# Kernel optimization log

Measured on AMD Instinct MI355X. Metric: run time of the kernel, lower is better.

The kernel has to match this reference:

```python
import jax, jax.numpy as jnp
import numpy as np

D_MODEL = 768
D_INNER = 1536      # d_model * expand
D_STATE = 128
D_CONV = 4
HEADDIM = 64
NHEADS = 24         # d_inner / headdim
CONV_DIM = D_INNER + 2 * D_STATE          # 1792
D_IN_PROJ = 2 * D_INNER + 2 * D_STATE + NHEADS  # 3352
EPS = 1e-5
BATCH, SEQLEN = 4, 2048


def setup_inputs() -> dict:
    key = jax.random.key(0)
    ks = jax.random.split(key, 8)
    u = jax.random.normal(ks[0], (BATCH, SEQLEN, D_MODEL), dtype=jnp.float32)
    W_in = jax.random.normal(ks[1], (D_IN_PROJ, D_MODEL), dtype=jnp.float32) * 0.02
    conv_w = jax.random.normal(ks[2], (CONV_DIM, D_CONV), dtype=jnp.float32) * 0.2
    conv_b = jnp.zeros((CONV_DIM,), dtype=jnp.float32)
    # dt_bias = inverse-softplus of dt sampled log-uniformly in [dt_min, dt_max]
    dt = jnp.exp(jax.random.uniform(ks[3], (NHEADS,)) * (np.log(0.1) - np.log(0.001)) + np.log(0.001))
    dt = jnp.clip(dt, 1e-4, None)
    dt_bias = dt + jnp.log(-jnp.expm1(-dt))
    A_log = jnp.log(jax.random.uniform(ks[4], (NHEADS,), minval=1.0, maxval=16.0))
    D = jnp.ones((NHEADS,), dtype=jnp.float32)
    norm_w = jnp.ones((D_INNER,), dtype=jnp.float32)
    W_out = jax.random.normal(ks[5], (D_MODEL, D_INNER), dtype=jnp.float32) * 0.02
    return {"u": u, "W_in": W_in, "conv_w": conv_w, "conv_b": conv_b,
            "dt_bias": dt_bias, "A_log": A_log, "D": D, "norm_w": norm_w, "W_out": W_out}


def reference(u, W_in, conv_w, conv_b, dt_bias, A_log, D, norm_w, W_out):
    b, L, _ = u.shape
    zxbcdt = jnp.einsum('bld,ed->ble', u, W_in)  # (b, L, 3352)
    z = zxbcdt[..., :D_INNER]
    xBC = zxbcdt[..., D_INNER:D_INNER + CONV_DIM]
    dt = zxbcdt[..., D_INNER + CONV_DIM:]        # (b, L, nheads)

    # causal depthwise conv1d (kernel width 4), then SiLU
    xp = jnp.pad(xBC, ((0, 0), (D_CONV - 1, 0), (0, 0)))
    xBC = sum(xp[:, k:k + L, :] * conv_w[:, k] for k in range(D_CONV)) + conv_b
    xBC = jax.nn.silu(xBC)

    x = xBC[..., :D_INNER].reshape(b, L, NHEADS, HEADDIM)
    B = xBC[..., D_INNER:D_INNER + D_STATE]      # (b, L, n)  (ngroups=1)
    C = xBC[..., D_INNER + D_STATE:]             # (b, L, n)

    dt = jax.nn.softplus(dt + dt_bias)           # (b, L, h)
    A = -jnp.exp(A_log)                          # (h,)
    dA = jnp.exp(dt * A)                         # (b, L, h)

    def step(h, inp):
        dA_t, dt_t, x_t, B_t, C_t = inp
        # h: (b, h, p, n)
        h = h * dA_t[:, :, None, None] + jnp.einsum('bhp,bh,bn->bhpn', x_t, dt_t, B_t)
        y = jnp.einsum('bhpn,bn->bhp', h, C_t)
        return h, y

    xs = (jnp.swapaxes(dA, 0, 1), jnp.swapaxes(dt, 0, 1), jnp.swapaxes(x, 0, 1),
          jnp.swapaxes(B, 0, 1), jnp.swapaxes(C, 0, 1))
    h0 = jnp.zeros((b, NHEADS, HEADDIM, D_STATE), dtype=u.dtype)
    _, ys = jax.lax.scan(step, h0, xs)           # ys: (L, b, h, p)
    y = jnp.swapaxes(ys, 0, 1)                   # (b, L, h, p)

    y = y + D[None, None, :, None] * x           # skip connection
    y = y.reshape(b, L, D_INNER)

    # RMSNorm then gate with silu(z)
    y = norm_w * y * jax.lax.rsqrt(jnp.mean(y * y, axis=-1, keepdims=True) + EPS)
    y = y * jax.nn.silu(z)
    return jnp.einsum('bld,ed->ble', y, W_out)
```

## Files before the change

kernel.cpp:

```cpp
#include <hip/hip_runtime.h>
#include <hip/hip_bf16.h>

typedef __bf16 bf16x8 __attribute__((ext_vector_type(8)));
typedef float f32x4 __attribute__((ext_vector_type(4)));
typedef unsigned int u32x4 __attribute__((ext_vector_type(4)));

#define MTOT    8192
#define DMODEL  768
#define DINNER  1536
#define DSTATE  128
#define NHEADS  24
#define CONVDIM 1792
#define LDZ     3328
#define SEQ     2048
#define CHUNK   128
#define NCHUNK  16
#define NBH     96

#define NU   (MTOT*DMODEL)
#define NWI  (LDZ*DMODEL)
#define NWO  (DMODEL*DINNER)
#define NWD  (32*DMODEL)

__device__ __forceinline__ void gl2lds16(const __hip_bfloat16* g, __hip_bfloat16* l) {
  __builtin_amdgcn_global_load_lds((const __attribute__((address_space(1))) void*)g,
                                   (__attribute__((address_space(3))) void*)l, 16, 0, 0);
}

__global__ __launch_bounds__(256) void cvt_bf16(const float* __restrict__ u, const float* __restrict__ Wi,
                                                const float* __restrict__ Wo,
                                                __hip_bfloat16* __restrict__ ub, __hip_bfloat16* __restrict__ wib,
                                                __hip_bfloat16* __restrict__ wob,
                                                __hip_bfloat16* __restrict__ wdh, __hip_bfloat16* __restrict__ wdl) {
  int i = blockIdx.x * 256 + threadIdx.x;
  if (i < NU) ub[i] = __float2bfloat16(u[i]);
  else if (i < NU + NWI) { int k = i - NU; wib[k] = __float2bfloat16(Wi[k]); }
  else if (i < NU + NWI + NWO) { int k = i - NU - NWI; wob[k] = __float2bfloat16(Wo[k]); }
  else if (i < NU + NWI + NWO + 2 * NWD) {
    int k = i - NU - NWI - NWO;
    int lo = (k >= NWD);
    if (lo) k -= NWD;
    int row = k / DMODEL, col = k - row * DMODEL;
    float w = (row < NHEADS) ? Wi[(size_t)(LDZ + row) * DMODEL + col] : 0.f;
    __hip_bfloat16 h = __float2bfloat16(w);
    if (!lo) wdh[k] = h;
    else wdl[k] = __float2bfloat16(w - __bfloat162float(h));
  }
}

__global__ __launch_bounds__(256, 2) void gemm_bt(const __hip_bfloat16* __restrict__ A,
                                                  const __hip_bfloat16* __restrict__ B,
                                                  float* __restrict__ C, int lda, int ldb, int ldc, int nk) {
  __shared__ __align__(16) __hip_bfloat16 As[128 * 32];
  __shared__ __align__(16) __hip_bfloat16 Bs[128 * 32];
  const int tid = threadIdx.x;
  const int lane = tid & 63, wid = tid >> 6;
  const int wm = wid >> 1, wn = wid & 1;
  const int bm = blockIdx.y, bn = blockIdx.x;
  const int sr = (lane >> 2), sc = (lane & 3) * 8;
  const __hip_bfloat16* Ag0 = A + (size_t)(bm * 128 + wid * 32 + sr) * lda + sc;
  const __hip_bfloat16* Ag1 = Ag0 + (size_t)16 * lda;
  const __hip_bfloat16* Bg0 = B + (size_t)(bn * 128 + wid * 32 + sr) * ldb + sc;
  const __hip_bfloat16* Bg1 = Bg0 + (size_t)16 * ldb;
  __hip_bfloat16* Al0 = &As[(wid * 32) * 32];
  __hip_bfloat16* Al1 = &As[(wid * 32 + 16) * 32];
  __hip_bfloat16* Bl0 = &Bs[(wid * 32) * 32];
  __hip_bfloat16* Bl1 = &Bs[(wid * 32 + 16) * 32];
  f32x4 acc[4][4] = {};
  const int lr = lane & 15, lk = lane >> 4;
  const int arow = wm * 64 + lr, brow = wn * 64 + lr;
  for (int ks = 0; ks < nk; ++ks) {
    gl2lds16(Ag0 + ks * 32, Al0);
    gl2lds16(Ag1 + ks * 32, Al1);
    gl2lds16(Bg0 + ks * 32, Bl0);
    gl2lds16(Bg1 + ks * 32, Bl1);
    __syncthreads();
    bf16x8 af[4], bfr[4];
#pragma unroll
    for (int i = 0; i < 4; ++i) {
      af[i] = *(const bf16x8*)&As[(arow + i * 16) * 32 + lk * 8];
      bfr[i] = *(const bf16x8*)&Bs[(brow + i * 16) * 32 + lk * 8];
    }
#pragma unroll
    for (int i = 0; i < 4; ++i)
#pragma unroll
      for (int j = 0; j < 4; ++j)
        acc[i][j] = __builtin_amdgcn_mfma_f32_16x16x32_bf16(af[i], bfr[j], acc[i][j], 0, 0, 0);
    __syncthreads();
  }
  const int crow0 = bm * 128 + wm * 64 + lk * 4;
  const int ccol0 = bn * 128 + wn * 64 + lr;
#pragma unroll
  for (int i = 0; i < 4; ++i)
#pragma unroll
    for (int j = 0; j < 4; ++j)
#pragma unroll
      for (int r = 0; r < 4; ++r)
        C[(size_t)(crow0 + i * 16 + r) * ldc + ccol0 + j * 16] = acc[i][j][r];
}

__global__ __launch_bounds__(256) void dt_mfma(const float* __restrict__ u,
                                               const __hip_bfloat16* __restrict__ wdh,
                                               const __hip_bfloat16* __restrict__ wdl,
                                               const float* __restrict__ dtb, const float* __restrict__ alog,
                                               float* __restrict__ dtS, float* __restrict__ dtA) {
  __shared__ __align__(16) __hip_bfloat16 Uh[64 * 32];
  __shared__ __align__(16) __hip_bfloat16 Ul[64 * 32];
  const int tid = threadIdx.x;
  const int lane = tid & 63, wid = tid >> 6;
  const int lr = lane & 15, lk = lane >> 4;
  const int bm = blockIdx.x;
  const int r = tid >> 2, c0 = (tid & 3) * 8;
  const float* usrc = u + (size_t)(bm * 64 + r) * DMODEL + c0;
  f32x4 acc[2] = {};
  for (int ks = 0; ks < DMODEL / 32; ++ks) {
    float4 v0 = *(const float4*)(usrc + ks * 32);
    float4 v1 = *(const float4*)(usrc + ks * 32 + 4);
    bf16x8 hi, lo;
    const float* vf = (const float*)&v0;
#pragma unroll
    for (int e = 0; e < 4; ++e) {
      __hip_bfloat16 h = __float2bfloat16(vf[e]);
      hi[e] = *(__bf16*)&h;
      __hip_bfloat16 l2 = __float2bfloat16(vf[e] - __bfloat162float(h));
      lo[e] = *(__bf16*)&l2;
    }
    vf = (const float*)&v1;
#pragma unroll
    for (int e = 0; e < 4; ++e) {
      __hip_bfloat16 h = __float2bfloat16(vf[e]);
      hi[4 + e] = *(__bf16*)&h;
      __hip_bfloat16 l2 = __float2bfloat16(vf[e] - __bfloat162float(h));
      lo[4 + e] = *(__bf16*)&l2;
    }
    *(bf16x8*)&Uh[r * 32 + c0] = hi;
    *(bf16x8*)&Ul[r * 32 + c0] = lo;
    __syncthreads();
    bf16x8 ah = *(const bf16x8*)&Uh[(wid * 16 + lr) * 32 + lk * 8];
    bf16x8 al = *(const bf16x8*)&Ul[(wid * 16 + lr) * 32 + lk * 8];
#pragma unroll
    for (int j = 0; j < 2; ++j) {
      bf16x8 bh = *(const bf16x8*)(wdh + (size_t)(j * 16 + lr) * DMODEL + ks * 32 + lk * 8);
      bf16x8 bl = *(const bf16x8*)(wdl + (size_t)(j * 16 + lr) * DMODEL + ks * 32 + lk * 8);
      acc[j] = __builtin_amdgcn_mfma_f32_16x16x32_bf16(ah, bh, acc[j], 0, 0, 0);
      acc[j] = __builtin_amdgcn_mfma_f32_16x16x32_bf16(ah, bl, acc[j], 0, 0, 0);
      acc[j] = __builtin_amdgcn_mfma_f32_16x16x32_bf16(al, bh, acc[j], 0, 0, 0);
    }
    __syncthreads();
  }
#pragma unroll
  for (int j = 0; j < 2; ++j) {
    int col = j * 16 + lr;
    if (col < NHEADS) {
      float nA = -expf(alog[col]);
      float bia = dtb[col];
#pragma unroll
      for (int rr = 0; rr < 4; ++rr) {
        int row = bm * 64 + wid * 16 + lk * 4 + rr;
        float x = acc[j][rr] + bia;
        float dt = (x > 20.f) ? x : log1pf(expf(x));
        dtS[(size_t)row * NHEADS + col] = dt;
        dtA[(size_t)row * NHEADS + col] = nA * dt;
      }
    }
  }
}

__global__ __launch_bounds__(256) void cumsum_kernel(const float* __restrict__ dtA, float* __restrict__ scum,
                                                     float* __restrict__ cdec) {
  int bc = blockIdx.x;
  int b = bc >> 4, c = bc & 15;
  __shared__ float buf[CHUNK * NHEADS];
  int m0 = b * SEQ + c * CHUNK;
  for (int t = threadIdx.x; t < CHUNK * NHEADS; t += 256)
    buf[t] = dtA[(size_t)m0 * NHEADS + t];
  __syncthreads();
  if (threadIdx.x < NHEADS) {
    int h = threadIdx.x;
    float run = 0.f;
    float* dst = scum + ((size_t)bc * NHEADS + h) * CHUNK;
    for (int j = 0; j < CHUNK; ++j) { run += buf[j * NHEADS + h]; dst[j] = run; }
    cdec[(b * NHEADS + h) * NCHUNK + c] = __expf(run);
  }
}

__global__ __launch_bounds__(256) void conv_prep(const float* __restrict__ zxb, const float* __restrict__ cw,
                                                 const float* __restrict__ cb, const float* __restrict__ dtS,
                                                 __hip_bfloat16* __restrict__ Xd, __hip_bfloat16* __restrict__ Bb,
                                                 __hip_bfloat16* __restrict__ Cb) {
  int c = blockIdx.x * 256 + threadIdx.x;
  int m = blockIdx.y;
  int l = m & (SEQ - 1);
  const float* src = zxb + (size_t)m * LDZ + DINNER + c;
  float4 w = *(const float4*)(cw + (size_t)c * 4);
  float acc = cb[c];
#pragma unroll
  for (int k = 0; k < 4; ++k) {
    int ll = l + k - 3;
    if (ll >= 0) acc = fmaf(src[(ptrdiff_t)(k - 3) * LDZ], ((const float*)&w)[k], acc);
  }
  float v = acc / (1.f + __expf(-acc));
  if (c < DINNER) Xd[(size_t)m * DINNER + c] = __float2bfloat16(dtS[m * NHEADS + (c >> 6)] * v);
  else if (c < DINNER + DSTATE) Bb[(size_t)m * DSTATE + (c - DINNER)] = __float2bfloat16(v);
  else Cb[(size_t)m * DSTATE + (c - DINNER - DSTATE)] = __float2bfloat16(v);
}

__global__ __launch_bounds__(256) void transp(const __hip_bfloat16* __restrict__ Xd,
                                              const __hip_bfloat16* __restrict__ Bb,
                                              __hip_bfloat16* __restrict__ XdT, __hip_bfloat16* __restrict__ Bt) {
  __shared__ __hip_bfloat16 t[64][72];
  int bid = blockIdx.x;
  const __hip_bfloat16* src;
  __hip_bfloat16* dst;
  int srcld;
  if (bid < 3072) {
    int tm = bid & 127, tc = bid >> 7;
    int m0 = tm * 64, c0 = tc * 64, b = m0 >> 11;
    src = Xd + (size_t)m0 * DINNER + c0; srcld = DINNER;
    dst = XdT + ((size_t)(b * DINNER + c0)) * SEQ + (m0 - b * SEQ);
  } else {
    int k = bid - 3072;
    int tm = k & 127, tn = k >> 7;
    int m0 = tm * 64, n0 = tn * 64, b = m0 >> 11;
    src = Bb + (size_t)m0 * DSTATE + n0; srcld = DSTATE;
    dst = Bt + ((size_t)(b * DSTATE + n0)) * SEQ + (m0 - b * SEQ);
  }
  int r = threadIdx.x >> 2, cc = (threadIdx.x & 3) * 16;
  *(u32x4*)&t[r][cc] = *(const u32x4*)(src + (size_t)r * srcld + cc);
  *(u32x4*)&t[r][cc + 8] = *(const u32x4*)(src + (size_t)r * srcld + cc + 8);
  __syncthreads();
  __hip_bfloat16 tmp[16] __attribute__((aligned(16)));
#pragma unroll
  for (int k2 = 0; k2 < 16; ++k2) tmp[k2] = t[cc + k2][r];
  *(u32x4*)(dst + (size_t)r * SEQ + cc) = *(u32x4*)&tmp[0];
  *(u32x4*)(dst + (size_t)r * SEQ + cc + 8) = *(u32x4*)&tmp[8];
}

__global__ __launch_bounds__(256, 2) void state_gemm(const __hip_bfloat16* __restrict__ XdT,
                                                     const __hip_bfloat16* __restrict__ Bt,
                                                     const float* __restrict__ scum, float* __restrict__ cstat) {
  __shared__ __align__(16) __hip_bfloat16 Xw[64 * 136];
  __shared__ __align__(16) __hip_bfloat16 Bts[128 * 136];
  __shared__ float rS[CHUNK];
  int bid = blockIdx.x;
  int c = bid & 15, bh = bid >> 4;
  int b = bh / NHEADS, h = bh % NHEADS;
  const float* sp = scum + ((size_t)(b * NCHUNK + c) * NHEADS + h) * CHUNK;
  int tid = threadIdx.x;
  if (tid < CHUNK) rS[tid] = __expf(sp[CHUNK - 1] - sp[tid]);
  {
    int n = tid >> 1, jc = (tid & 1) * 64;
    const __hip_bfloat16* g = Bt + ((size_t)(b * DSTATE + n)) * SEQ + c * CHUNK + jc;
#pragma unroll
    for (int q = 0; q < 8; ++q) *(u32x4*)&Bts[n * 136 + jc + q * 8] = *(const u32x4*)(g + q * 8);
  }
  __syncthreads();
  {
    int p = tid >> 2, jc = (tid & 3) * 32;
    const __hip_bfloat16* g = XdT + ((size_t)((b * NHEADS + h) * 64 + p)) * SEQ + c * CHUNK + jc;
#pragma unroll
    for (int q = 0; q < 4; ++q) {
      bf16x8 vv = *(const bf16x8*)(g + q * 8);
      bf16x8 ov;
#pragma unroll
      for (int e = 0; e < 8; ++e) ov[e] = (__bf16)((float)vv[e] * rS[jc + q * 8 + e]);
      *(bf16x8*)&Xw[p * 136 + jc + q * 8] = ov;
    }
  }
  __syncthreads();
  const int lane = tid & 63, wid = tid >> 6;
  const int wm = wid >> 1, wn = wid & 1;
  const int lr = lane & 15, lk = lane >> 4;
  f32x4 acc[2][4] = {};
#pragma unroll
  for (int ks = 0; ks < 4; ++ks) {
    bf16x8 af[2], bq[4];
#pragma unroll
    for (int i = 0; i < 2; ++i) af[i] = *(const bf16x8*)&Xw[(wm * 32 + i * 16 + lr) * 136 + ks * 32 + lk * 8];
#pragma unroll
    for (int j = 0; j < 4; ++j) bq[j] = *(const bf16x8*)&Bts[(wn * 64 + j * 16 + lr) * 136 + ks * 32 + lk * 8];
#pragma unroll
    for (int i = 0; i < 2; ++i)
#pragma unroll
      for (int j = 0; j < 4; ++j)
        acc[i][j] = __builtin_amdgcn_mfma_f32_16x16x32_bf16(af[i], bq[j], acc[i][j], 0, 0, 0);
  }
  float* dst = cstat + (size_t)bid * 8192;
#pragma unroll
  for (int i = 0; i < 2; ++i)
#pragma unroll
    for (int j = 0; j < 4; ++j)
#pragma unroll
      for (int r = 0; r < 4; ++r)
        dst[(wm * 32 + i * 16 + lk * 4 + r) * 128 + wn * 64 + j * 16 + lr] = acc[i][j][r];
}

__global__ __launch_bounds__(256) void scanB(float* __restrict__ cstat, const float* __restrict__ cdec) {
  const int bh = blockIdx.x >> 3, sl = blockIdx.x & 7;
  const int base = sl * 1024 + threadIdx.x * 4;
  float hreg[4];
#pragma unroll
  for (int j = 0; j < 4; ++j) hreg[j] = 0.f;
  for (int c = 0; c < NCHUNK; ++c) {
    float* p = cstat + (size_t)(bh * NCHUNK + c) * 8192 + base;
    const float P = cdec[bh * NCHUNK + c];
    f32x4 tmp = *(const f32x4*)p;
    f32x4 hs = {hreg[0], hreg[1], hreg[2], hreg[3]};
    *(f32x4*)p = hs;
#pragma unroll
    for (int j = 0; j < 4; ++j) hreg[j] = fmaf(hreg[j], P, tmp[j]);
  }
}

template <int JE>
__global__ __launch_bounds__(256, 2) void ssd_y(const __hip_bfloat16* __restrict__ Cb,
                                                const __hip_bfloat16* __restrict__ Bb,
                                                const __hip_bfloat16* __restrict__ XdT,
                                                const __hip_bfloat16* __restrict__ Xd,
                                                const float* __restrict__ cstat, const float* __restrict__ scum,
                                                const float* __restrict__ dtS, const float* __restrict__ Dvec,
                                                float* __restrict__ zxb) {
  constexpr int HI = JE - 64;
  constexpr int JW = JE / 2;
  constexpr int FJ = JW / 16;
  constexpr int KJ = JE / 32;
  __shared__ __align__(16) __hip_bfloat16 Cs[64 * 136];
  __shared__ __align__(16) __hip_bfloat16 Bs[JE * 136];
  __shared__ __align__(16) __hip_bfloat16 R3[64 * 136];
  __shared__ float sS[CHUNK];
  int bid = blockIdx.x;
  int c = bid & 15, bh = bid >> 4;
  int b = bh / NHEADS, h = bh % NHEADS;
  int m0 = b * SEQ + c * CHUNK;
  int tid = threadIdx.x;
  const float* sp = scum + ((size_t)(b * NCHUNK + c) * NHEADS + h) * CHUNK;
  if (tid < CHUNK) sS[tid] = sp[tid];
  {
    int r = tid >> 2, nc = (tid & 3) * 32;
    const __hip_bfloat16* g = Cb + (size_t)(m0 + HI + r) * DSTATE + nc;
#pragma unroll
    for (int q = 0; q < 4; ++q) *(u32x4*)&Cs[r * 136 + nc + q * 8] = *(const u32x4*)(g + q * 8);
  }
  if (JE == 64) {
    int r = tid >> 2, nc = (tid & 3) * 32;
    const __hip_bfloat16* g = Bb + (size_t)(m0 + r) * DSTATE + nc;
#pragma unroll
    for (int q = 0; q < 4; ++q) *(u32x4*)&Bs[r * 136 + nc + q * 8] = *(const u32x4*)(g + q * 8);
  } else {
    int r = tid >> 1, nc = (tid & 1) * 64;
    const __hip_bfloat16* g = Bb + (size_t)(m0 + r) * DSTATE + nc;
#pragma unroll
    for (int q = 0; q < 8; ++q) *(u32x4*)&Bs[r * 136 + nc + q * 8] = *(const u32x4*)(g + q * 8);
  }
  {
    int p = tid >> 2, nc = (tid & 3) * 32;
    const float* g = cstat + (size_t)bid * 8192 + p * 128 + nc;
#pragma unroll
    for (int q = 0; q < 4; ++q) {
      f32x4 v0 = *(const f32x4*)(g + q * 8);
      f32x4 v1 = *(const f32x4*)(g + q * 8 + 4);
      bf16x8 ov;
      ov[0] = (__bf16)v0[0]; ov[1] = (__bf16)v0[1]; ov[2] = (__bf16)v0[2]; ov[3] = (__bf16)v0[3];
      ov[4] = (__bf16)v1[0]; ov[5] = (__bf16)v1[1]; ov[6] = (__bf16)v1[2]; ov[7] = (__bf16)v1[3];
      *(bf16x8*)&R3[p * 136 + nc + q * 8] = ov;
    }
  }
  __syncthreads();
  const int lane = tid & 63, wid = tid >> 6;
  const int wm = wid >> 1, wn = wid & 1;
  const int lr = lane & 15, lk = lane >> 4;
  f32x4 Gacc[2][FJ] = {};
  f32x4 Uacc[2][2] = {};
#pragma unroll
  for (int ks = 0; ks < 4; ++ks) {
    bf16x8 af[2], bq[2];
#pragma unroll
    for (int i = 0; i < 2; ++i) af[i] = *(const bf16x8*)&Cs[(wm * 32 + i * 16 + lr) * 136 + ks * 32 + lk * 8];
#pragma unroll
    for (int j = 0; j < 2; ++j) bq[j] = *(const bf16x8*)&R3[(wn * 32 + j * 16 + lr) * 136 + ks * 32 + lk * 8];
#pragma unroll
    for (int i = 0; i < 2; ++i)
#pragma unroll
      for (int j = 0; j < 2; ++j)
        Uacc[i][j] = __builtin_amdgcn_mfma_f32_16x16x32_bf16(af[i], bq[j], Uacc[i][j], 0, 0, 0);
  }
#pragma unroll
  for (int ks = 0; ks < 4; ++ks) {
    bf16x8 af[2], bq[FJ];
#pragma unroll
    for (int i = 0; i < 2; ++i) af[i] = *(const bf16x8*)&Cs[(wm * 32 + i * 16 + lr) * 136 + ks * 32 + lk * 8];
#pragma unroll
    for (int j = 0; j < FJ; ++j) bq[j] = *(const bf16x8*)&Bs[(wn * JW + j * 16 + lr) * 136 + ks * 32 + lk * 8];
#pragma unroll
    for (int i = 0; i < 2; ++i)
#pragma unroll
      for (int j = 0; j < FJ; ++j)
        Gacc[i][j] = __builtin_amdgcn_mfma_f32_16x16x32_bf16(af[i], bq[j], Gacc[i][j], 0, 0, 0);
  }
  __syncthreads();
  {
    float siv[2][4];
#pragma unroll
    for (int i = 0; i < 2; ++i)
#pragma unroll
      for (int r = 0; r < 4; ++r) siv[i][r] = sS[HI + wm * 32 + i * 16 + lk * 4 + r];
#pragma unroll
    for (int i = 0; i < 2; ++i)
#pragma unroll
      for (int j = 0; j < FJ; ++j) {
        int gj = wn * JW + j * 16 + lr;
        float sj = sS[gj];
#pragma unroll
        for (int r = 0; r < 4; ++r) {
          int il = wm * 32 + i * 16 + lk * 4 + r;
          int gi = HI + il;
          float mv = (gj <= gi) ? Gacc[i][j][r] * __expf(siv[i][r] - sj) : 0.f;
          Cs[il * 136 + gj] = __float2bfloat16(mv);
        }
      }
  }
  {
    int p = tid >> 2, jc = (tid & 3) * (JE / 4);
    const __hip_bfloat16* g = XdT + ((size_t)((b * NHEADS + h) * 64 + p)) * SEQ + c * CHUNK + jc;
#pragma unroll
    for (int q = 0; q < JE / 32; ++q) *(u32x4*)&R3[p * 136 + jc + q * 8] = *(const u32x4*)(g + q * 8);
  }
  __syncthreads();
  f32x4 Yacc[2][2] = {};
#pragma unroll
  for (int ks = 0; ks < KJ; ++ks) {
    bf16x8 af[2], bq[2];
#pragma unroll
    for (int i = 0; i < 2; ++i) af[i] = *(const bf16x8*)&Cs[(wm * 32 + i * 16 + lr) * 136 + ks * 32 + lk * 8];
#pragma unroll
    for (int j = 0; j < 2; ++j) bq[j] = *(const bf16x8*)&R3[(wn * 32 + j * 16 + lr) * 136 + ks * 32 + lk * 8];
#pragma unroll
    for (int i = 0; i < 2; ++i)
#pragma unroll
      for (int j = 0; j < 2; ++j)
        Yacc[i][j] = __builtin_amdgcn_mfma_f32_16x16x32_bf16(af[i], bq[j], Yacc[i][j], 0, 0, 0);
  }
  const float Dh = Dvec[h];
#pragma unroll
  for (int i = 0; i < 2; ++i)
#pragma unroll
    for (int r = 0; r < 4; ++r) {
      int il = wm * 32 + i * 16 + lk * 4 + r;
      int gi = HI + il;
      int m = m0 + gi;
      float ei = __expf(sS[gi]);
      float dt = dtS[(size_t)m * NHEADS + h];
#pragma unroll
      for (int j = 0; j < 2; ++j) {
        int p = wn * 32 + j * 16 + lr;
        float xv = (float)Xd[(size_t)m * DINNER + h * 64 + p] / dt;
        zxb[(size_t)m * LDZ + DINNER + h * 64 + p] = Yacc[i][j][r] + ei * Uacc[i][j][r] + Dh * xv;
      }
    }
}

__global__ __launch_bounds__(256) void norm_gate(const float* __restrict__ zxb, const float* __restrict__ nw,
                                                 __hip_bfloat16* __restrict__ yg) {
  const int m = blockIdx.x, tid = threadIdx.x;
  const float* zr = zxb + (size_t)m * LDZ;
  const float* yr = zr + DINNER;
  float yv[6], zv[6];
  float ss = 0.f;
#pragma unroll
  for (int jj = 0; jj < 6; ++jj) {
    int i = tid + jj * 256;
    yv[jj] = yr[i];
    zv[jj] = zr[i];
    ss = fmaf(yv[jj], yv[jj], ss);
  }
#pragma unroll
  for (int o = 32; o > 0; o >>= 1) ss += __shfl_down(ss, o);
  __shared__ float red[4];
  if ((tid & 63) == 0) red[tid >> 6] = ss;
  __syncthreads();
  float tot = red[0] + red[1] + red[2] + red[3];
  float r = rsqrtf(tot * (1.f / 1536.f) + 1e-5f);
#pragma unroll
  for (int jj = 0; jj < 6; ++jj) {
    int i = tid + jj * 256;
    float z = zv[jj];
    float g = z / (1.f + __expf(-z));
    yg[(size_t)m * DINNER + i] = __float2bfloat16(nw[i] * yv[jj] * r * g);
  }
}

extern "C" void kernel_launch(void* const* d_in, const int* in_sizes, int n_in,
                              void* d_out, int out_size, void* d_ws, size_t ws_size,
                              hipStream_t stream) {
  (void)in_sizes; (void)n_in; (void)out_size; (void)ws_size;
  const float* u       = (const float*)d_in[0];
  const float* W_in    = (const float*)d_in[1];
  const float* conv_w  = (const float*)d_in[2];
  const float* conv_b  = (const float*)d_in[3];
  const float* dt_bias = (const float*)d_in[4];
  const float* A_log   = (const float*)d_in[5];
  const float* Dvec    = (const float*)d_in[6];
  const float* norm_w  = (const float*)d_in[7];
  const float* W_out   = (const float*)d_in[8];
  float* out = (float*)d_out;

  float* zxb   = (float*)d_ws;
  float* cstat = zxb + (size_t)MTOT * LDZ;
  float* dtS   = cstat + (size_t)NBH * NCHUNK * 8192;
  float* dtA   = dtS + (size_t)MTOT * NHEADS;
  float* scum  = dtA + (size_t)MTOT * NHEADS;
  float* cdec  = scum + (size_t)MTOT * NHEADS;
  __hip_bfloat16* ub  = (__hip_bfloat16*)(cdec + NBH * NCHUNK);
  __hip_bfloat16* wib = ub + (size_t)NU;
  __hip_bfloat16* wob = wib + (size_t)NWI;
  __hip_bfloat16* wdh = wob + (size_t)NWO;
  __hip_bfloat16* wdl = wdh + (size_t)NWD;
  __hip_bfloat16* Xd  = wdl + (size_t)NWD;
  __hip_bfloat16* Bb  = Xd + (size_t)MTOT * DINNER;
  __hip_bfloat16* Cb  = Bb + (size_t)MTOT * DSTATE;
  __hip_bfloat16* XdT = Cb + (size_t)MTOT * DSTATE;
  __hip_bfloat16* Bt  = XdT + (size_t)MTOT * DINNER;
  __hip_bfloat16* yg  = Xd;

  cvt_bf16<<<(NU + NWI + NWO + 2 * NWD + 255) / 256, 256, 0, stream>>>(u, W_in, W_out, ub, wib, wob, wdh, wdl);
  gemm_bt<<<dim3(LDZ / 128, MTOT / 128), 256, 0, stream>>>(ub, wib, zxb, DMODEL, DMODEL, LDZ, DMODEL / 32);
  dt_mfma<<<MTOT / 64, 256, 0, stream>>>(u, wdh, wdl, dt_bias, A_log, dtS, dtA);
  cumsum_kernel<<<64, 256, 0, stream>>>(dtA, scum, cdec);
  conv_prep<<<dim3(CONVDIM / 256, MTOT), 256, 0, stream>>>(zxb, conv_w, conv_b, dtS, Xd, Bb, Cb);
  transp<<<3072 + 256, 256, 0, stream>>>(Xd, Bb, XdT, Bt);
  state_gemm<<<NBH * NCHUNK, 256, 0, stream>>>(XdT, Bt, scum, cstat);
  scanB<<<NBH * 8, 256, 0, stream>>>(cstat, cdec);
  ssd_y<64><<<NBH * NCHUNK, 256, 0, stream>>>(Cb, Bb, XdT, Xd, cstat, scum, dtS, Dvec, zxb);
  ssd_y<128><<<NBH * NCHUNK, 256, 0, stream>>>(Cb, Bb, XdT, Xd, cstat, scum, dtS, Dvec, zxb);
  norm_gate<<<MTOT, 256, 0, stream>>>(zxb, norm_w, yg);
  gemm_bt<<<dim3(DMODEL / 128, MTOT / 128), 256, 0, stream>>>(yg, wob, out, DINNER, DINNER, DMODEL, DINNER / 32);
}
```

Before: 416.7 us.

## Double-buffer GEMM LDS with swizzle, fuse conv with transpose, store chunk states in bf16

The bf16 GEMM now double-buffers its LDS tiles, issuing the next k-step's global-to-LDS loads before the current MFMAs, and XOR-swizzles the tile layout to reduce bank conflicts. The conv/SiLU kernel is merged with the transpose kernel, so each 64x64 tile is computed once, written row-major and transposed from LDS, which removes a launch and a re-read of Xd/Bb. Per-chunk states are stored in bf16 instead of fp32, halving traffic through state_gemm, scanB and ssd_y. The trade-off is extra rounding in the inter-chunk state recurrence, and twice the GEMM LDS footprint, which may limit occupancy.

```diff
diff --git a/kernel.cpp b/kernel.cpp
--- a/kernel.cpp
+++ b/kernel.cpp
@@ -51,35 +51,40 @@
 __global__ __launch_bounds__(256, 2) void gemm_bt(const __hip_bfloat16* __restrict__ A,
                                                   const __hip_bfloat16* __restrict__ B,
                                                   float* __restrict__ C, int lda, int ldb, int ldc, int nk) {
-  __shared__ __align__(16) __hip_bfloat16 As[128 * 32];
-  __shared__ __align__(16) __hip_bfloat16 Bs[128 * 32];
+  __shared__ __align__(16) __hip_bfloat16 As[2][128 * 32];
+  __shared__ __align__(16) __hip_bfloat16 Bs[2][128 * 32];
   const int tid = threadIdx.x;
   const int lane = tid & 63, wid = tid >> 6;
   const int wm = wid >> 1, wn = wid & 1;
   const int bm = blockIdx.y, bn = blockIdx.x;
-  const int sr = (lane >> 2), sc = (lane & 3) * 8;
-  const __hip_bfloat16* Ag0 = A + (size_t)(bm * 128 + wid * 32 + sr) * lda + sc;
+  const int sr = lane >> 2;
+  const int sc = (((lane & 3) ^ ((sr >> 1) & 3))) * 8;
+  const int row0 = wid * 32 + sr;
+  const __hip_bfloat16* Ag0 = A + (size_t)(bm * 128 + row0) * lda + sc;
   const __hip_bfloat16* Ag1 = Ag0 + (size_t)16 * lda;
-  const __hip_bfloat16* Bg0 = B + (size_t)(bn * 128 + wid * 32 + sr) * ldb + sc;
+  const __hip_bfloat16* Bg0 = B + (size_t)(bn * 128 + row0) * ldb + sc;
   const __hip_bfloat16* Bg1 = Bg0 + (size_t)16 * ldb;
-  __hip_bfloat16* Al0 = &As[(wid * 32) * 32];
-  __hip_bfloat16* Al1 = &As[(wid * 32 + 16) * 32];
-  __hip_bfloat16* Bl0 = &Bs[(wid * 32) * 32];
-  __hip_bfloat16* Bl1 = &Bs[(wid * 32 + 16) * 32];
   f32x4 acc[4][4] = {};
   const int lr = lane & 15, lk = lane >> 4;
   const int arow = wm * 64 + lr, brow = wn * 64 + lr;
+  const int ach = (lk ^ ((lr >> 1) & 3)) * 8;
+#define STAGE(buf, ks)                                   \
+  do {                                                   \
+    gl2lds16(Ag0 + (ks) * 32, &As[buf][(wid * 32) * 32]);      \
+    gl2lds16(Ag1 + (ks) * 32, &As[buf][(wid * 32 + 16) * 32]); \
+    gl2lds16(Bg0 + (ks) * 32, &Bs[buf][(wid * 32) * 32]);      \
+    gl2lds16(Bg1 + (ks) * 32, &Bs[buf][(wid * 32 + 16) * 32]); \
+  } while (0)
+  STAGE(0, 0);
+  __syncthreads();
   for (int ks = 0; ks < nk; ++ks) {
-    gl2lds16(Ag0 + ks * 32, Al0);
-    gl2lds16(Ag1 + ks * 32, Al1);
-    gl2lds16(Bg0 + ks * 32, Bl0);
-    gl2lds16(Bg1 + ks * 32, Bl1);
-    __syncthreads();
+    const int cur = ks & 1;
+    if (ks + 1 < nk) STAGE(cur ^ 1, ks + 1);
     bf16x8 af[4], bfr[4];
 #pragma unroll
     for (int i = 0; i < 4; ++i) {
-      af[i] = *(const bf16x8*)&As[(arow + i * 16) * 32 + lk * 8];
-      bfr[i] = *(const bf16x8*)&Bs[(brow + i * 16) * 32 + lk * 8];
+      af[i] = *(const bf16x8*)&As[cur][(arow + i * 16) * 32 + ach];
+      bfr[i] = *(const bf16x8*)&Bs[cur][(brow + i * 16) * 32 + ach];
     }
 #pragma unroll
     for (int i = 0; i < 4; ++i)
@@ -88,6 +93,7 @@
         acc[i][j] = __builtin_amdgcn_mfma_f32_16x16x32_bf16(af[i], bfr[j], acc[i][j], 0, 0, 0);
     __syncthreads();
   }
+#undef STAGE
   const int crow0 = bm * 128 + wm * 64 + lk * 4;
   const int ccol0 = bn * 128 + wn * 64 + lr;
 #pragma unroll
@@ -184,61 +190,59 @@
   }
 }
 
-__global__ __launch_bounds__(256) void conv_prep(const float* __restrict__ zxb, const float* __restrict__ cw,
-                                                 const float* __restrict__ cb, const float* __restrict__ dtS,
-                                                 __hip_bfloat16* __restrict__ Xd, __hip_bfloat16* __restrict__ Bb,
-                                                 __hip_bfloat16* __restrict__ Cb) {
-  int c = blockIdx.x * 256 + threadIdx.x;
-  int m = blockIdx.y;
-  int l = m & (SEQ - 1);
-  const float* src = zxb + (size_t)m * LDZ + DINNER + c;
-  float4 w = *(const float4*)(cw + (size_t)c * 4);
-  float acc = cb[c];
-#pragma unroll
-  for (int k = 0; k < 4; ++k) {
-    int ll = l + k - 3;
-    if (ll >= 0) acc = fmaf(src[(ptrdiff_t)(k - 3) * LDZ], ((const float*)&w)[k], acc);
-  }
-  float v = acc / (1.f + __expf(-acc));
-  if (c < DINNER) Xd[(size_t)m * DINNER + c] = __float2bfloat16(dtS[m * NHEADS + (c >> 6)] * v);
-  else if (c < DINNER + DSTATE) Bb[(size_t)m * DSTATE + (c - DINNER)] = __float2bfloat16(v);
-  else Cb[(size_t)m * DSTATE + (c - DINNER - DSTATE)] = __float2bfloat16(v);
-}
-
-__global__ __launch_bounds__(256) void transp(const __hip_bfloat16* __restrict__ Xd,
-                                              const __hip_bfloat16* __restrict__ Bb,
-                                              __hip_bfloat16* __restrict__ XdT, __hip_bfloat16* __restrict__ Bt) {
+__global__ __launch_bounds__(256) void conv_fused(const float* __restrict__ zxb, const float* __restrict__ cw,
+                                                  const float* __restrict__ cb, const float* __restrict__ dtS,
+                                                  __hip_bfloat16* __restrict__ Xd, __hip_bfloat16* __restrict__ Bb,
+                                                  __hip_bfloat16* __restrict__ Cb, __hip_bfloat16* __restrict__ XdT,
+                                                  __hip_bfloat16* __restrict__ Bt) {
   __shared__ __hip_bfloat16 t[64][72];
-  int bid = blockIdx.x;
-  const __hip_bfloat16* src;
-  __hip_bfloat16* dst;
-  int srcld;
-  if (bid < 3072) {
-    int tm = bid & 127, tc = bid >> 7;
-    int m0 = tm * 64, c0 = tc * 64, b = m0 >> 11;
-    src = Xd + (size_t)m0 * DINNER + c0; srcld = DINNER;
-    dst = XdT + ((size_t)(b * DINNER + c0)) * SEQ + (m0 - b * SEQ);
-  } else {
-    int k = bid - 3072;
-    int tm = k & 127, tn = k >> 7;
-    int m0 = tm * 64, n0 = tn * 64, b = m0 >> 11;
-    src = Bb + (size_t)m0 * DSTATE + n0; srcld = DSTATE;
-    dst = Bt + ((size_t)(b * DSTATE + n0)) * SEQ + (m0 - b * SEQ);
-  }
-  int r = threadIdx.x >> 2, cc = (threadIdx.x & 3) * 16;
-  *(u32x4*)&t[r][cc] = *(const u32x4*)(src + (size_t)r * srcld + cc);
-  *(u32x4*)&t[r][cc + 8] = *(const u32x4*)(src + (size_t)r * srcld + cc + 8);
-  __syncthreads();
-  __hip_bfloat16 tmp[16] __attribute__((aligned(16)));
-#pragma unroll
-  for (int k2 = 0; k2 < 16; ++k2) tmp[k2] = t[cc + k2][r];
-  *(u32x4*)(dst + (size_t)r * SEQ + cc) = *(u32x4*)&tmp[0];
-  *(u32x4*)(dst + (size_t)r * SEQ + cc + 8) = *(u32x4*)&tmp[8];
+  __shared__ float dts_sh[64];
+  const int c0 = blockIdx.x * 64, m0 = blockIdx.y * 64;
+  const int b = m0 >> 11, l0 = m0 & (SEQ - 1);
+  const int tid = threadIdx.x;
+  const int c = tid & 63, rg = tid >> 6;
+  const int gc = c0 + c;
+  const bool isX = (c0 < DINNER);
+  if (isX && tid < 64) dts_sh[tid] = dtS[(size_t)(m0 + tid) * NHEADS + (c0 >> 6)];
+  const float4 w = *(const float4*)(cw + (size_t)gc * 4);
+  const float bias = cb[gc];
+  const float* src = zxb + (size_t)(m0 + rg * 16) * LDZ + DINNER + gc;
+  const int lbase = l0 + rg * 16;
+  float v0 = (lbase >= 3) ? src[-3 * (ptrdiff_t)LDZ] : 0.f;
+  float v1 = (lbase >= 2) ? src[-2 * (ptrdiff_t)LDZ] : 0.f;
+  float v2 = (lbase >= 1) ? src[-1 * (ptrdiff_t)LDZ] : 0.f;
+  __syncthreads();
+#pragma unroll
+  for (int r = 0; r < 16; ++r) {
+    float v3 = src[(ptrdiff_t)r * LDZ];
+    float a = bias + v0 * w.x + v1 * w.y + v2 * w.z + v3 * w.w;
+    float sv = a / (1.f + __expf(-a));
+    int lm = rg * 16 + r;
+    __hip_bfloat16 val = __float2bfloat16(isX ? dts_sh[lm] * sv : sv);
+    t[lm][c] = val;
+    int m = m0 + lm;
+    if (isX) Xd[(size_t)m * DINNER + gc] = val;
+    else if (gc < DINNER + DSTATE) Bb[(size_t)m * DSTATE + gc - DINNER] = val;
+    else Cb[(size_t)m * DSTATE + gc - DINNER - DSTATE] = val;
+    v0 = v1; v1 = v2; v2 = v3;
+  }
+  __syncthreads();
+  if (c0 < DINNER + DSTATE) {
+    int r2 = tid >> 2, cc = (tid & 3) * 16;
+    __hip_bfloat16 tmp[16] __attribute__((aligned(16)));
+#pragma unroll
+    for (int k = 0; k < 16; ++k) tmp[k] = t[cc + k][r2];
+    __hip_bfloat16* dst = isX ? XdT + ((size_t)(b * DINNER + c0 + r2)) * SEQ + l0 + cc
+                              : Bt + ((size_t)(b * DSTATE + (c0 - DINNER) + r2)) * SEQ + l0 + cc;
+    *(u32x4*)dst = *(u32x4*)&tmp[0];
+    *(u32x4*)(dst + 8) = *(u32x4*)&tmp[8];
+  }
 }
 
 __global__ __launch_bounds__(256, 2) void state_gemm(const __hip_bfloat16* __restrict__ XdT,
                                                      const __hip_bfloat16* __restrict__ Bt,
-                                                     const float* __restrict__ scum, float* __restrict__ cstat) {
+                                                     const float* __restrict__ scum,
+                                                     __hip_bfloat16* __restrict__ cstat) {
   __shared__ __align__(16) __hip_bfloat16 Xw[64 * 136];
   __shared__ __align__(16) __hip_bfloat16 Bts[128 * 136];
   __shared__ float rS[CHUNK];
@@ -285,30 +289,30 @@
       for (int j = 0; j < 4; ++j)
         acc[i][j] = __builtin_amdgcn_mfma_f32_16x16x32_bf16(af[i], bq[j], acc[i][j], 0, 0, 0);
   }
-  float* dst = cstat + (size_t)bid * 8192;
+  __hip_bfloat16* dst = cstat + (size_t)bid * 8192;
 #pragma unroll
   for (int i = 0; i < 2; ++i)
 #pragma unroll
     for (int j = 0; j < 4; ++j)
 #pragma unroll
       for (int r = 0; r < 4; ++r)
-        dst[(wm * 32 + i * 16 + lk * 4 + r) * 128 + wn * 64 + j * 16 + lr] = acc[i][j][r];
-}
-
-__global__ __launch_bounds__(256) void scanB(float* __restrict__ cstat, const float* __restrict__ cdec) {
+        dst[(wm * 32 + i * 16 + lk * 4 + r) * 128 + wn * 64 + j * 16 + lr] = __float2bfloat16(acc[i][j][r]);
+}
+
+__global__ __launch_bounds__(256) void scanB(__hip_bfloat16* __restrict__ cstat, const float* __restrict__ cdec) {
   const int bh = blockIdx.x >> 3, sl = blockIdx.x & 7;
   const int base = sl * 1024 + threadIdx.x * 4;
-  float hreg[4];
-#pragma unroll
-  for (int j = 0; j < 4; ++j) hreg[j] = 0.f;
+  float hreg[4] = {0.f, 0.f, 0.f, 0.f};
   for (int c = 0; c < NCHUNK; ++c) {
-    float* p = cstat + (size_t)(bh * NCHUNK + c) * 8192 + base;
+    __hip_bfloat16* p = cstat + (size_t)(bh * NCHUNK + c) * 8192 + base;
     const float P = cdec[bh * NCHUNK + c];
-    f32x4 tmp = *(const f32x4*)p;
-    f32x4 hs = {hreg[0], hreg[1], hreg[2], hreg[3]};
-    *(f32x4*)p = hs;
-#pragma unroll
-    for (int j = 0; j < 4; ++j) hreg[j] = fmaf(hreg[j], P, tmp[j]);
+    __hip_bfloat16 tmp[4], hs[4];
+    *(uint2*)tmp = *(const uint2*)p;
+#pragma unroll
+    for (int j = 0; j < 4; ++j) hs[j] = __float2bfloat16(hreg[j]);
+    *(uint2*)p = *(uint2*)hs;
+#pragma unroll
+    for (int j = 0; j < 4; ++j) hreg[j] = fmaf(hreg[j], P, __bfloat162float(tmp[j]));
   }
 }
 
@@ -317,7 +321,8 @@
                                                 const __hip_bfloat16* __restrict__ Bb,
                                                 const __hip_bfloat16* __restrict__ XdT,
                                                 const __hip_bfloat16* __restrict__ Xd,
-                                                const float* __restrict__ cstat, const float* __restrict__ scum,
+                                                const __hip_bfloat16* __restrict__ cstat,
+                                                const float* __restrict__ scum,
                                                 const float* __restrict__ dtS, const float* __restrict__ Dvec,
                                                 float* __restrict__ zxb) {
   constexpr int HI = JE - 64;
@@ -354,16 +359,9 @@
   }
   {
     int p = tid >> 2, nc = (tid & 3) * 32;
-    const float* g = cstat + (size_t)bid * 8192 + p * 128 + nc;
-#pragma unroll
-    for (int q = 0; q < 4; ++q) {
-      f32x4 v0 = *(const f32x4*)(g + q * 8);
-      f32x4 v1 = *(const f32x4*)(g + q * 8 + 4);
-      bf16x8 ov;
-      ov[0] = (__bf16)v0[0]; ov[1] = (__bf16)v0[1]; ov[2] = (__bf16)v0[2]; ov[3] = (__bf16)v0[3];
-      ov[4] = (__bf16)v1[0]; ov[5] = (__bf16)v1[1]; ov[6] = (__bf16)v1[2]; ov[7] = (__bf16)v1[3];
-      *(bf16x8*)&R3[p * 136 + nc + q * 8] = ov;
-    }
+    const __hip_bfloat16* g = cstat + (size_t)bid * 8192 + p * 128 + nc;
+#pragma unroll
+    for (int q = 0; q < 4; ++q) *(u32x4*)&R3[p * 136 + nc + q * 8] = *(const u32x4*)(g + q * 8);
   }
   __syncthreads();
   const int lane = tid & 63, wid = tid >> 6;
@@ -504,12 +502,12 @@
   const float* W_out   = (const float*)d_in[8];
   float* out = (float*)d_out;
 
-  float* zxb   = (float*)d_ws;
-  float* cstat = zxb + (size_t)MTOT * LDZ;
-  float* dtS   = cstat + (size_t)NBH * NCHUNK * 8192;
-  float* dtA   = dtS + (size_t)MTOT * NHEADS;
-  float* scum  = dtA + (size_t)MTOT * NHEADS;
-  float* cdec  = scum + (size_t)MTOT * NHEADS;
+  float* zxb = (float*)d_ws;
+  __hip_bfloat16* cstatb = (__hip_bfloat16*)(zxb + (size_t)MTOT * LDZ);
+  float* dtS  = (float*)(cstatb + (size_t)NBH * NCHUNK * 8192);
+  float* dtA  = dtS + (size_t)MTOT * NHEADS;
+  float* scum = dtA + (size_t)MTOT * NHEADS;
+  float* cdec = scum + (size_t)MTOT * NHEADS;
   __hip_bfloat16* ub  = (__hip_bfloat16*)(cdec + NBH * NCHUNK);
   __hip_bfloat16* wib = ub + (size_t)NU;
   __hip_bfloat16* wob = wib + (size_t)NWI;
@@ -526,12 +524,11 @@
   gemm_bt<<<dim3(LDZ / 128, MTOT / 128), 256, 0, stream>>>(ub, wib, zxb, DMODEL, DMODEL, LDZ, DMODEL / 32);
   dt_mfma<<<MTOT / 64, 256, 0, stream>>>(u, wdh, wdl, dt_bias, A_log, dtS, dtA);
   cumsum_kernel<<<64, 256, 0, stream>>>(dtA, scum, cdec);
-  conv_prep<<<dim3(CONVDIM / 256, MTOT), 256, 0, stream>>>(zxb, conv_w, conv_b, dtS, Xd, Bb, Cb);
-  transp<<<3072 + 256, 256, 0, stream>>>(Xd, Bb, XdT, Bt);
-  state_gemm<<<NBH * NCHUNK, 256, 0, stream>>>(XdT, Bt, scum, cstat);
-  scanB<<<NBH * 8, 256, 0, stream>>>(cstat, cdec);
-  ssd_y<64><<<NBH * NCHUNK, 256, 0, stream>>>(Cb, Bb, XdT, Xd, cstat, scum, dtS, Dvec, zxb);
-  ssd_y<128><<<NBH * NCHUNK, 256, 0, stream>>>(Cb, Bb, XdT, Xd, cstat, scum, dtS, Dvec, zxb);
+  conv_fused<<<dim3(CONVDIM / 64, MTOT / 64), 256, 0, stream>>>(zxb, conv_w, conv_b, dtS, Xd, Bb, Cb, XdT, Bt);
+  state_gemm<<<NBH * NCHUNK, 256, 0, stream>>>(XdT, Bt, scum, cstatb);
+  scanB<<<NBH * 8, 256, 0, stream>>>(cstatb, cdec);
+  ssd_y<64><<<NBH * NCHUNK, 256, 0, stream>>>(Cb, Bb, XdT, Xd, cstatb, scum, dtS, Dvec, zxb);
+  ssd_y<128><<<NBH * NCHUNK, 256, 0, stream>>>(Cb, Bb, XdT, Xd, cstatb, scum, dtS, Dvec, zxb);
   norm_gate<<<MTOT, 256, 0, stream>>>(zxb, norm_w, yg);
   gemm_bt<<<dim3(DMODEL / 128, MTOT / 128), 256, 0, stream>>>(yg, wob, out, DINNER, DINNER, DMODEL, DINNER / 32);
 }
```

New measurement: 350.1 us. -16.0%, faster.
